# Optimization experiments

Hardware: AMD Instinct MI355X
Metric: run time of the kernel (lower is better)

The kernel has to match this reference:

```python
import jax, jax.numpy as jnp
import numpy as np

B, NQ, ISIZE = 8, 2048, 1024
H, D, NA = 8, 128, 8            # num_head, attn_dim, num_anchor
AH = H * D                      # ahsize = 1024
ASZ = NA * D                    # anchor_size = 1024
FH = 4096                       # _fhsize
ISZ_NET = FH * H // NA          # 4096, input dim of self.net
EPS = 1e-6


def setup_inputs() -> dict:
    key = jax.random.key(0)
    ks = jax.random.split(key, 12)
    def u(k, shape, fan_in):
        s = 1.0 / np.sqrt(fan_in)
        return jax.random.uniform(k, shape, jnp.float32, -s, s)
    return {
        "inputs": jax.random.normal(ks[0], (B, NQ, ISIZE), jnp.float32),
        "ln_g": jnp.ones((ISIZE,), jnp.float32),
        "ln_b": jnp.zeros((ISIZE,), jnp.float32),
        "q_anchor": u(ks[1], (H, NA, D), D),
        "W_qkv": u(ks[2], (ISIZE, 3 * AH), ISIZE), "b_qkv": jnp.zeros((3 * AH,), jnp.float32),
        "W_an": u(ks[3], (ASZ, FH), ASZ), "b_an": jnp.zeros((FH,), jnp.float32),
        "W_n1": u(ks[4], (ISZ_NET, AH), ISZ_NET), "b_n1": jnp.zeros((AH,), jnp.float32),
        "W_n2": u(ks[5], (AH, FH), AH), "b_n2": jnp.zeros((FH,), jnp.float32),
        "W_n3": u(ks[6], (FH, AH), FH), "b_n3": jnp.zeros((AH,), jnp.float32),
        "W_k": u(ks[7], (AH, AH), AH), "b_k": jnp.zeros((AH,), jnp.float32),
        "W_o": u(ks[8], (AH, ISIZE), AH), "b_o": jnp.zeros((ISIZE,), jnp.float32),
    }


def reference(inputs, ln_g, ln_b, q_anchor, W_qkv, b_qkv, W_an, b_an,
              W_n1, b_n1, W_n2, b_n2, W_n3, b_n3, W_k, b_k, W_o, b_o):
    b, nq = inputs.shape[:2]
    scale = 1.0 / np.sqrt(D)
    # pre-LayerNorm
    mu = jnp.mean(inputs, -1, keepdims=True)
    var = jnp.mean(jnp.square(inputs - mu), -1, keepdims=True)
    x = (inputs - mu) * jax.lax.rsqrt(var + EPS) * ln_g + ln_b
    # QKV projection
    qkv = (x @ W_qkv + b_qkv).reshape(b, nq, 3, H, D)
    q = jnp.transpose(qkv[:, :, 0], (0, 2, 1, 3))   # [b,H,nq,D]
    k = qkv[:, :, 1]                                  # [b,nq,H,D]
    v = qkv[:, :, 2]                                  # [b,nq,H,D]
    # stage 1: fixed anchors attend over the sequence
    sc1 = jax.nn.softmax(jnp.einsum('had,bnhd->bhan', q_anchor, k) * scale, axis=-1)
    out = jnp.einsum('bhan,bnhd->bhad', sc1, v).reshape(b, H, ASZ)   # [b,H,NA*D]
    # anchor_net (share_head Linear + ReLU)
    out = jax.nn.relu(out @ W_an + b_an)                              # [b,H,FH]
    # regroup head-major -> anchor-major
    out = out.reshape(b, H, NA, FH // NA).transpose(0, 2, 1, 3).reshape(b, NA, ISZ_NET)
    # net: bottleneck Linear -> Linear -> ReLU -> Linear
    out = jax.nn.relu((out @ W_n1 + b_n1) @ W_n2 + b_n2) @ W_n3 + b_n3  # [b,NA,AH]
    # stage 2: queries attend over anchors
    kk = (out @ W_k + b_k).reshape(b, NA, H, D)
    sc2 = jax.nn.softmax(jnp.einsum('bhqd,bahd->bhqa', q, kk) * scale, axis=-1)
    ov = out.reshape(b, NA, H, D)
    y = jnp.einsum('bhqa,bahd->bqhd', sc2, ov).reshape(b, nq, AH)
    return y @ W_o + b_o + inputs
```

## Files before the change

### kernel.cpp

```cpp
#include <hip/hip_runtime.h>
#include <cstdint>
#include <cstddef>

typedef unsigned short u16;
typedef __attribute__((ext_vector_type(8))) short short8;
typedef __attribute__((ext_vector_type(4))) float floatx4;
typedef __attribute__((ext_vector_type(16))) float floatx16;

__device__ __forceinline__ u16 f2bf(float f) {
  unsigned u = __float_as_uint(f);
  u += 0x7fffu + ((u >> 16) & 1u);
  return (u16)(u >> 16);
}
__device__ __forceinline__ float bf2f(u16 s) {
  return __uint_as_float(((unsigned)s) << 16);
}

__global__ __launch_bounds__(256) void ln_kernel(const float* __restrict__ x,
                                                 const float* __restrict__ g,
                                                 const float* __restrict__ bta,
                                                 u16* __restrict__ out) {
  const int row = blockIdx.x;
  const int tid = threadIdx.x;
  const float4 v = ((const float4*)(x + (size_t)row * 1024))[tid];
  float s = v.x + v.y + v.z + v.w;
#pragma unroll
  for (int o = 32; o > 0; o >>= 1) s += __shfl_down(s, o);
  __shared__ float red[4], red2[4];
  const int wv = tid >> 6, ln = tid & 63;
  if (ln == 0) red[wv] = s;
  __syncthreads();
  const float mean = (red[0] + red[1] + red[2] + red[3]) * (1.0f / 1024.0f);
  const float dx = v.x - mean, dy = v.y - mean, dz = v.z - mean, dw = v.w - mean;
  float s2 = dx * dx + dy * dy + dz * dz + dw * dw;
#pragma unroll
  for (int o = 32; o > 0; o >>= 1) s2 += __shfl_down(s2, o);
  if (ln == 0) red2[wv] = s2;
  __syncthreads();
  const float var = (red2[0] + red2[1] + red2[2] + red2[3]) * (1.0f / 1024.0f);
  const float rstd = rsqrtf(var + 1e-6f);
  const float4 gg = ((const float4*)g)[tid];
  const float4 bb = ((const float4*)bta)[tid];
  ushort4 o4;
  o4.x = f2bf(dx * rstd * gg.x + bb.x);
  o4.y = f2bf(dy * rstd * gg.y + bb.y);
  o4.z = f2bf(dz * rstd * gg.z + bb.z);
  o4.w = f2bf(dw * rstd * gg.w + bb.w);
  ((ushort4*)(out + (size_t)row * 1024))[tid] = o4;
}

__global__ __launch_bounds__(256) void transpose_bf16(const float* __restrict__ W,
                                                      u16* __restrict__ WT,
                                                      int K, int N) {
  __shared__ float t[32][33];
  const int kb = blockIdx.x * 32, nb = blockIdx.y * 32;
  const int tx = threadIdx.x & 31, ty = threadIdx.x >> 5;
#pragma unroll
  for (int i = ty; i < 32; i += 8) t[i][tx] = W[(size_t)(kb + i) * N + nb + tx];
  __syncthreads();
#pragma unroll
  for (int i = ty; i < 32; i += 8) WT[(size_t)(nb + i) * K + kb + tx] = f2bf(t[tx][i]);
}


__device__ __forceinline__ void stageG(const u16* __restrict__ gp, u16* lp, int K) {
  __builtin_amdgcn_global_load_lds((const __attribute__((address_space(1))) void*)gp,
                                   (__attribute__((address_space(3))) void*)lp, 16, 0, 0);
  __builtin_amdgcn_global_load_lds((const __attribute__((address_space(1))) void*)(gp + ((size_t)K << 6)),
                                   (__attribute__((address_space(3))) void*)(lp + 4096), 16, 0, 0);
}

__device__ __forceinline__ void rdA(short8 (&af)[2][4], const u16* sbuf, const int (&ab)[4],
                                    int halfoff) {
#pragma unroll
  for (int mi = 0; mi < 2; ++mi)
#pragma unroll
    for (int ks = 0; ks < 4; ++ks)
      af[mi][ks] = *(const short8*)(sbuf + halfoff + mi * 2048 + ab[ks]);
}
__device__ __forceinline__ void rdB(short8 (&bf)[4], const u16* sbuf, const int (&bb)[4],
                                    int halfoff) {
#pragma unroll
  for (int ks = 0; ks < 4; ++ks)
    bf[ks] = *(const short8*)(sbuf + halfoff + bb[ks]);
}

template <int Q>
__device__ __forceinline__ void mfmaQ(floatx16 (&acc)[4][2], const short8 (&af)[2][4],
                                      const short8 (&bf)[4]) {
#pragma unroll
  for (int ks = 0; ks < 4; ++ks)
#pragma unroll
    for (int mi = 0; mi < 2; ++mi)
      acc[Q][mi] = __builtin_amdgcn_mfma_f32_32x32x16_bf16(af[mi][ks], bf[ks], acc[Q][mi], 0, 0, 0);
}

template <int B_>
__device__ __forceinline__ void gtile(int t, int NT, int K,
                                      u16 (&sA)[2][16384], u16 (&sB)[2][16384],
                                      const u16* gA_lo, const u16* gA_hi,
                                      const u16* gB_lo, const u16* gB_hi,
                                      u16* ldsA_cur, u16* ldsA_alt,
                                      u16* ldsB_cur, u16* ldsB_alt,
                                      const int (&ab)[4], const int (&bb)[4],
                                      floatx16 (&acc)[4][2]) {
  short8 af[2][4], bf0[4], bf1[4];
  rdA(af, sA[B_], ab, 0);
  rdB(bf0, sB[B_], bb, 0);
  __builtin_amdgcn_sched_barrier(0);
  if (t + 1 < NT) stageG(gA_hi + ((t + 1) << 6), ldsA_alt + 8192, K);
  rdB(bf1, sB[B_], bb, 8192);
  asm volatile("s_waitcnt lgkmcnt(4)" ::: "memory");
  __builtin_amdgcn_sched_barrier(0);
  __builtin_amdgcn_s_setprio(1);
  mfmaQ<0>(acc, af, bf0);
  __builtin_amdgcn_s_setprio(0);
  if (t + 1 < NT) stageG(gB_lo + ((t + 1) << 6), ldsB_alt, K);
  asm volatile("s_waitcnt lgkmcnt(0)" ::: "memory");
  __builtin_amdgcn_sched_barrier(0);
  __builtin_amdgcn_s_setprio(1);
  mfmaQ<1>(acc, af, bf1);
  __builtin_amdgcn_s_setprio(0);
  rdA(af, sA[B_], ab, 8192);
  __builtin_amdgcn_s_barrier();
  if (t + 2 < NT) stageG(gA_lo + ((t + 2) << 6), ldsA_cur, K);
  asm volatile("s_waitcnt lgkmcnt(0)" ::: "memory");
  __builtin_amdgcn_sched_barrier(0);
  __builtin_amdgcn_s_setprio(1);
  mfmaQ<2>(acc, af, bf1);
  __builtin_amdgcn_s_setprio(0);
  if (t + 2 < NT) stageG(gB_hi + ((t + 2) << 6), ldsB_cur + 8192, K);
  __builtin_amdgcn_s_setprio(1);
  mfmaQ<3>(acc, af, bf0);
  __builtin_amdgcn_s_setprio(0);
  if (t + 2 < NT) {
    asm volatile("s_waitcnt vmcnt(4)" ::: "memory");
  } else {
    asm volatile("s_waitcnt vmcnt(0)" ::: "memory");
  }
  __builtin_amdgcn_s_barrier();
}

template <int EPI>
__global__ __launch_bounds__(512, 2) void gemm_bf16(const u16* __restrict__ A,
                                                    const u16* __restrict__ BT,
                                                    const float* __restrict__ bias,
                                                    const float* __restrict__ extra,
                                                    u16* __restrict__ outB,
                                                    float* __restrict__ outF,
                                                    int M, int N, int K) {
  __shared__ u16 sA[2][16384];
  __shared__ u16 sB[2][16384];
  const int tid = threadIdx.x;
  const int wave = tid >> 6, lane = tid & 63;
  const int m0 = blockIdx.x * 256, n0 = blockIdx.y * 256;
  const int wr = wave >> 2, wc = wave & 3;
  const int l31 = lane & 31, l5 = lane >> 5, l7 = lane & 7;
  const int NT = K >> 6;

  int ab[4], bb[4];
#pragma unroll
  for (int ks = 0; ks < 4; ++ks) {
    const int xr = ((((ks << 1) + l5) ^ l7) << 3);
    ab[ks] = (wr * 64 + l31) * 64 + xr;
    bb[ks] = (wc * 32 + l31) * 64 + xr;
  }
  const int srow = wave * 8 + (lane >> 3);
  const int scol = ((lane & 7) ^ (srow & 7)) << 3;
  const u16* gA_lo = A + (size_t)(m0 + srow) * K + scol;
  const u16* gA_hi = A + (size_t)(m0 + 128 + srow) * K + scol;
  const u16* gB_lo = BT + (size_t)(n0 + srow) * K + scol;
  const u16* gB_hi = BT + (size_t)(n0 + 128 + srow) * K + scol;

  floatx16 acc[4][2];
#pragma unroll
  for (int q = 0; q < 4; ++q)
#pragma unroll
    for (int mi = 0; mi < 2; ++mi)
#pragma unroll
      for (int r = 0; r < 16; ++r) acc[q][mi][r] = 0.f;

  stageG(gA_lo, &sA[0][0] + wave * 512, K);
  stageG(gA_hi, &sA[0][8192] + wave * 512, K);
  stageG(gB_lo, &sB[0][0] + wave * 512, K);
  stageG(gB_hi, &sB[0][8192] + wave * 512, K);
  stageG(gA_lo + 64, &sA[1][0] + wave * 512, K);
  stageG(gB_hi + 64, &sB[1][8192] + wave * 512, K);
  asm volatile("s_waitcnt vmcnt(4)" ::: "memory");
  __builtin_amdgcn_s_barrier();

  for (int t = 0; t < NT; t += 2) {
    gtile<0>(t, NT, K, sA, sB, gA_lo, gA_hi, gB_lo, gB_hi,
             &sA[0][0] + wave * 512, &sA[1][0] + wave * 512,
             &sB[0][0] + wave * 512, &sB[1][0] + wave * 512, ab, bb, acc);
    gtile<1>(t + 1, NT, K, sA, sB, gA_lo, gA_hi, gB_lo, gB_hi,
             &sA[1][0] + wave * 512, &sA[0][0] + wave * 512,
             &sB[1][0] + wave * 512, &sB[0][0] + wave * 512, ab, bb, acc);
  }

#pragma unroll
  for (int q = 0; q < 4; ++q) {
    const int QM = q >> 1, QN = QM ^ (q & 1);
    const int n = n0 + QN * 128 + wc * 32 + l31;
    const float bs = bias[n];
#pragma unroll
    for (int mi = 0; mi < 2; ++mi) {
      const int mb = m0 + QM * 128 + wr * 64 + mi * 32 + 4 * l5;
#pragma unroll
      for (int reg = 0; reg < 16; ++reg) {
        const int m = mb + (reg & 3) + 8 * (reg >> 2);
        const float v = acc[q][mi][reg] + bs;
        if (EPI == 0)
          outB[(size_t)m * N + n] = f2bf(v);
        else
          outF[(size_t)m * N + n] = v + extra[(size_t)m * N + n];
      }
    }
  }
}

__global__ __launch_bounds__(256) void attn1_scores(const u16* __restrict__ qkv,
                                                    const float* __restrict__ q_anchor,
                                                    float* __restrict__ S) {
  __shared__ float qa[8][128];
  const int tid = threadIdx.x;
  const int chunk = blockIdx.x & 7, bh = blockIdx.x >> 3;
  const int b = bh >> 3, h = bh & 7;
  for (int i = tid; i < 1024; i += 256) qa[i >> 7][i & 127] = q_anchor[h * 1024 + i];
  __syncthreads();
  const float scale = 0.0883883476483184f;
  const int n = chunk * 256 + tid;
  const u16* kp = qkv + (size_t)(b * 2048 + n) * 3072 + 1024 + h * 128;
  float dots[8] = {0, 0, 0, 0, 0, 0, 0, 0};
#pragma unroll 8
  for (int dd = 0; dd < 128; dd += 4) {
    const ushort4 k4 = *(const ushort4*)(kp + dd);
    const float k0 = bf2f(k4.x), k1 = bf2f(k4.y), k2 = bf2f(k4.z), k3 = bf2f(k4.w);
#pragma unroll
    for (int a = 0; a < 8; ++a) {
      const float4 q4 = *(const float4*)&qa[a][dd];
      dots[a] += q4.x * k0 + q4.y * k1 + q4.z * k2 + q4.w * k3;
    }
  }
#pragma unroll
  for (int a = 0; a < 8; ++a) S[((size_t)(bh * 8 + a)) * 2048 + n] = dots[a] * scale;
}

__global__ __launch_bounds__(256) void attn1_softmax(float* __restrict__ S) {
  const int row = blockIdx.x;
  const int tid = threadIdx.x;
  float* Sp = S + (size_t)row * 2048;
  float4 v0 = ((const float4*)Sp)[tid * 2];
  float4 v1 = ((const float4*)Sp)[tid * 2 + 1];
  float mx = fmaxf(fmaxf(fmaxf(v0.x, v0.y), fmaxf(v0.z, v0.w)),
                   fmaxf(fmaxf(v1.x, v1.y), fmaxf(v1.z, v1.w)));
#pragma unroll
  for (int o = 32; o > 0; o >>= 1) mx = fmaxf(mx, __shfl_xor(mx, o));
  __shared__ float red[4];
  const int wv = tid >> 6, ln = tid & 63;
  if (ln == 0) red[wv] = mx;
  __syncthreads();
  mx = fmaxf(fmaxf(red[0], red[1]), fmaxf(red[2], red[3]));
  v0.x = __expf(v0.x - mx); v0.y = __expf(v0.y - mx);
  v0.z = __expf(v0.z - mx); v0.w = __expf(v0.w - mx);
  v1.x = __expf(v1.x - mx); v1.y = __expf(v1.y - mx);
  v1.z = __expf(v1.z - mx); v1.w = __expf(v1.w - mx);
  float sum = v0.x + v0.y + v0.z + v0.w + v1.x + v1.y + v1.z + v1.w;
#pragma unroll
  for (int o = 32; o > 0; o >>= 1) sum += __shfl_xor(sum, o);
  __shared__ float red2[4];
  if (ln == 0) red2[wv] = sum;
  __syncthreads();
  const float inv = 1.f / (red2[0] + red2[1] + red2[2] + red2[3]);
  v0.x *= inv; v0.y *= inv; v0.z *= inv; v0.w *= inv;
  v1.x *= inv; v1.y *= inv; v1.z *= inv; v1.w *= inv;
  ((float4*)Sp)[tid * 2] = v0;
  ((float4*)Sp)[tid * 2 + 1] = v1;
}

__global__ __launch_bounds__(256) void attn1_pv(const u16* __restrict__ qkv,
                                                const float* __restrict__ S,
                                                float* __restrict__ pvpart) {
  __shared__ float P[8][256];
  const int tid = threadIdx.x;
  const int chunk = blockIdx.x & 7, bh = blockIdx.x >> 3;
  const int b = bh >> 3, h = bh & 7;
  for (int i = tid; i < 2048; i += 256) {
    const int a = i >> 8, n = i & 255;
    P[a][n] = S[((size_t)(bh * 8 + a)) * 2048 + chunk * 256 + n];
  }
  __syncthreads();
  const int d = tid & 127, half = tid >> 7;
  const int nbase = chunk * 256 + half * 128;
  const u16* vp = qkv + (size_t)(b * 2048 + nbase) * 3072 + 2048 + h * 128 + d;
  float acc[8] = {0.f};
  for (int n = 0; n < 128; n += 4) {
    const float v0 = bf2f(vp[(size_t)n * 3072]);
    const float v1 = bf2f(vp[(size_t)(n + 1) * 3072]);
    const float v2 = bf2f(vp[(size_t)(n + 2) * 3072]);
    const float v3 = bf2f(vp[(size_t)(n + 3) * 3072]);
#pragma unroll
    for (int a = 0; a < 8; ++a) {
      const float4 s4 = *(const float4*)&P[a][half * 128 + n];
      acc[a] += s4.x * v0 + s4.y * v1 + s4.z * v2 + s4.w * v3;
    }
  }
  const int split = chunk * 2 + half;
#pragma unroll
  for (int a = 0; a < 8; ++a)
    pvpart[((size_t)split * 64 + bh) * 1024 + a * 128 + d] = acc[a];
}

__global__ __launch_bounds__(256) void mlp_mfma(const float* __restrict__ A,
                                                const float* __restrict__ W,
                                                float* __restrict__ part,
                                                int K, int N, int KC) {
  __shared__ float sW[64][33];
  const int tid = threadIdx.x;
  const int lane = tid & 63, wave = tid >> 6;
  const int wm = wave * 16;
  const int n0 = blockIdx.x * 64;
  const int kbeg = blockIdx.y * KC;
  const int l15 = lane & 15, kq8 = (lane >> 4) * 8;
  const int arow = wm + l15;

  floatx4 acc[4];
  const floatx4 zero = {0.f, 0.f, 0.f, 0.f};
#pragma unroll
  for (int j = 0; j < 4; ++j) acc[j] = zero;

  for (int kc = 0; kc < KC; kc += 32) {
    const int kbase = kbeg + kc;
    __syncthreads();
#pragma unroll
    for (int p = 0; p < 8; ++p) {
      const int k = p * 4 + wave;
      sW[lane][k] = W[(size_t)(kbase + k) * N + n0 + lane];
    }
    const float* ap = A + (size_t)arow * K + kbase + kq8;
    const float4 a0 = *(const float4*)ap;
    const float4 a1 = *(const float4*)(ap + 4);
    short8 af;
    af[0] = (short)f2bf(a0.x); af[1] = (short)f2bf(a0.y);
    af[2] = (short)f2bf(a0.z); af[3] = (short)f2bf(a0.w);
    af[4] = (short)f2bf(a1.x); af[5] = (short)f2bf(a1.y);
    af[6] = (short)f2bf(a1.z); af[7] = (short)f2bf(a1.w);
    __syncthreads();
#pragma unroll
    for (int j = 0; j < 4; ++j) {
      const float* wp = &sW[j * 16 + l15][kq8];
      short8 bf;
      bf[0] = (short)f2bf(wp[0]); bf[1] = (short)f2bf(wp[1]);
      bf[2] = (short)f2bf(wp[2]); bf[3] = (short)f2bf(wp[3]);
      bf[4] = (short)f2bf(wp[4]); bf[5] = (short)f2bf(wp[5]);
      bf[6] = (short)f2bf(wp[6]); bf[7] = (short)f2bf(wp[7]);
      acc[j] = __builtin_amdgcn_mfma_f32_16x16x32_bf16(af, bf, acc[j], 0, 0, 0);
    }
  }
  const int q = lane >> 4;
#pragma unroll
  for (int j = 0; j < 4; ++j)
#pragma unroll
    for (int r = 0; r < 4; ++r) {
      const int m = wm + q * 4 + r;
      const int n = n0 + j * 16 + l15;
      part[((size_t)blockIdx.y * 64 + m) * N + n] = acc[j][r];
    }
}

__global__ __launch_bounds__(256) void mlp_reduce(const float* __restrict__ part,
                                                  const float* __restrict__ bias,
                                                  float* __restrict__ out,
                                                  int N, int nsplit, int relu, int perm) {
  const int idx = blockIdx.x * 256 + threadIdx.x;
  const int e = idx * 4;
  if (e >= 64 * N) return;
  const int row = e / N, col = e - row * N;
  float4 acc;
  if (bias) acc = *(const float4*)&bias[col];
  else { acc.x = 0.f; acc.y = 0.f; acc.z = 0.f; acc.w = 0.f; }
  for (int s = 0; s < nsplit; ++s) {
    const float4 p = *(const float4*)&part[((size_t)s * 64 + row) * N + col];
    acc.x += p.x; acc.y += p.y; acc.z += p.z; acc.w += p.w;
  }
  if (relu) {
    acc.x = fmaxf(acc.x, 0.f); acc.y = fmaxf(acc.y, 0.f);
    acc.z = fmaxf(acc.z, 0.f); acc.w = fmaxf(acc.w, 0.f);
  }
  size_t oidx;
  if (!perm) {
    oidx = (size_t)row * N + col;
  } else {
    const int b = row >> 3, h = row & 7;
    oidx = (size_t)(b * 8 + (col >> 9)) * 4096 + h * 512 + (col & 511);
  }
  *(float4*)&out[oidx] = acc;
}

__global__ __launch_bounds__(256) void attn2_kernel(const u16* __restrict__ qkv,
                                                    const float* __restrict__ kk,
                                                    const float* __restrict__ onet,
                                                    u16* __restrict__ y) {
  __shared__ float kkl[8][128];
  __shared__ float ovl[8][128];
  const int tid = threadIdx.x;
  const int chunk = blockIdx.x & 7, bh = blockIdx.x >> 3;
  const int b = bh >> 3, h = bh & 7;
  for (int i = tid; i < 1024; i += 256) {
    const int a = i >> 7, d = i & 127;
    kkl[a][d] = kk[(size_t)(b * 8 + a) * 1024 + h * 128 + d];
    ovl[a][d] = onet[(size_t)(b * 8 + a) * 1024 + h * 128 + d];
  }
  __syncthreads();
  const int n = chunk * 256 + tid;
  const u16* qp = qkv + (size_t)(b * 2048 + n) * 3072 + h * 128;
  float dots[8] = {0, 0, 0, 0, 0, 0, 0, 0};
#pragma unroll 4
  for (int dd = 0; dd < 128; dd += 4) {
    const ushort4 q4 = *(const ushort4*)(qp + dd);
    const float q0 = bf2f(q4.x), q1 = bf2f(q4.y), q2 = bf2f(q4.z), q3 = bf2f(q4.w);
#pragma unroll
    for (int a = 0; a < 8; ++a) {
      const float4 k4 = *(const float4*)&kkl[a][dd];
      dots[a] += k4.x * q0 + k4.y * q1 + k4.z * q2 + k4.w * q3;
    }
  }
  const float scale = 0.0883883476483184f;
  float mx = -1e30f;
#pragma unroll
  for (int a = 0; a < 8; ++a) {
    dots[a] *= scale;
    mx = fmaxf(mx, dots[a]);
  }
  float p[8];
  float sum = 0.f;
#pragma unroll
  for (int a = 0; a < 8; ++a) {
    p[a] = __expf(dots[a] - mx);
    sum += p[a];
  }
  const float inv = 1.f / sum;
#pragma unroll
  for (int a = 0; a < 8; ++a) p[a] *= inv;
  u16* yp = y + (size_t)(b * 2048 + n) * 1024 + h * 128;
#pragma unroll 4
  for (int dd = 0; dd < 128; dd += 4) {
    float a0 = 0, a1 = 0, a2 = 0, a3 = 0;
#pragma unroll
    for (int a = 0; a < 8; ++a) {
      const float4 o4 = *(const float4*)&ovl[a][dd];
      a0 += p[a] * o4.x;
      a1 += p[a] * o4.y;
      a2 += p[a] * o4.z;
      a3 += p[a] * o4.w;
    }
    ushort4 o;
    o.x = f2bf(a0);
    o.y = f2bf(a1);
    o.z = f2bf(a2);
    o.w = f2bf(a3);
    *(ushort4*)(yp + dd) = o;
  }
}

extern "C" void kernel_launch(void* const* d_in, const int* in_sizes, int n_in,
                              void* d_out, int out_size, void* d_ws, size_t ws_size,
                              hipStream_t stream) {
  const float* inputs = (const float*)d_in[0];
  const float* ln_g = (const float*)d_in[1];
  const float* ln_b = (const float*)d_in[2];
  const float* q_anchor = (const float*)d_in[3];
  const float* W_qkv = (const float*)d_in[4];
  const float* b_qkv = (const float*)d_in[5];
  const float* W_an = (const float*)d_in[6];
  const float* b_an = (const float*)d_in[7];
  const float* W_n1 = (const float*)d_in[8];
  const float* b_n1 = (const float*)d_in[9];
  const float* W_n2 = (const float*)d_in[10];
  const float* b_n2 = (const float*)d_in[11];
  const float* W_n3 = (const float*)d_in[12];
  const float* b_n3 = (const float*)d_in[13];
  const float* W_k = (const float*)d_in[14];
  const float* b_k = (const float*)d_in[15];
  const float* W_o = (const float*)d_in[16];
  const float* b_o = (const float*)d_in[17];
  float* out = (float*)d_out;

  char* ws = (char*)d_ws;
  u16* qkv = (u16*)(ws);
  u16* xbf = (u16*)(ws + 100663296);
  float* S = (float*)(ws + 100663296);
  float* part = (float*)(ws + 109051904);
  u16* WqkvT = (u16*)(ws + 134217728);
  u16* WoT = (u16*)(ws + 140509184);
  float* att1 = (float*)(ws + 142606336);
  float* anp = (float*)(ws + 142868480);
  float* h1 = (float*)(ws + 143917056);
  float* h2 = (float*)(ws + 144179200);
  float* onet = (float*)(ws + 145227776);
  float* kkb = (float*)(ws + 145489920);

  ln_kernel<<<16384, 256, 0, stream>>>(inputs, ln_g, ln_b, xbf);
  transpose_bf16<<<dim3(32, 96), 256, 0, stream>>>(W_qkv, WqkvT, 1024, 3072);
  transpose_bf16<<<dim3(32, 32), 256, 0, stream>>>(W_o, WoT, 1024, 1024);
  gemm_bf16<0><<<dim3(64, 12), 512, 0, stream>>>(xbf, WqkvT, b_qkv, nullptr, qkv, nullptr,
                                                 16384, 3072, 1024);
  attn1_scores<<<512, 256, 0, stream>>>(qkv, q_anchor, S);
  attn1_softmax<<<512, 256, 0, stream>>>(S);
  attn1_pv<<<512, 256, 0, stream>>>(qkv, S, part);
  mlp_reduce<<<64, 256, 0, stream>>>(part, nullptr, att1, 1024, 16, 0, 0);
  mlp_mfma<<<dim3(64, 8), 256, 0, stream>>>(att1, W_an, part, 1024, 4096, 128);
  mlp_reduce<<<256, 256, 0, stream>>>(part, b_an, anp, 4096, 8, 1, 1);
  mlp_mfma<<<dim3(16, 32), 256, 0, stream>>>(anp, W_n1, part, 4096, 1024, 128);
  mlp_reduce<<<64, 256, 0, stream>>>(part, b_n1, h1, 1024, 32, 0, 0);
  mlp_mfma<<<dim3(64, 8), 256, 0, stream>>>(h1, W_n2, part, 1024, 4096, 128);
  mlp_reduce<<<256, 256, 0, stream>>>(part, b_n2, h2, 4096, 8, 1, 0);
  mlp_mfma<<<dim3(16, 32), 256, 0, stream>>>(h2, W_n3, part, 4096, 1024, 128);
  mlp_reduce<<<64, 256, 0, stream>>>(part, b_n3, onet, 1024, 32, 0, 0);
  mlp_mfma<<<dim3(16, 16), 256, 0, stream>>>(onet, W_k, part, 1024, 1024, 64);
  mlp_reduce<<<64, 256, 0, stream>>>(part, b_k, kkb, 1024, 16, 0, 0);
  attn2_kernel<<<512, 256, 0, stream>>>(qkv, kkb, onet, xbf);
  gemm_bf16<1><<<dim3(64, 4), 512, 0, stream>>>(xbf, WoT, b_o, inputs, nullptr, out,
                                                16384, 1024, 1024);
}
```

Measured before the change: 601.3 us.

## Change LDS swizzle and prefetch next tile's B fragments across the barrier

The GEMM's LDS XOR swizzle now also folds in the wave index and row group, with a per-mi XOR on A reads, to reduce bank conflicts on the ds_read paths. The main loop also carries B fragments across iterations: the low-half B fragments of the next tile are read after the barrier and before the last MFMA quarter. The two B register sets swap roles between tiles, so the reads overlap with compute instead of stalling at the start of each tile. This raises register pressure and depends on the staged writes and swizzled reads agreeing exactly.

```diff
diff --git a/kernel.cpp b/kernel.cpp
--- a/kernel.cpp
+++ b/kernel.cpp
@@ -76,7 +76,7 @@
   for (int mi = 0; mi < 2; ++mi)
 #pragma unroll
     for (int ks = 0; ks < 4; ++ks)
-      af[mi][ks] = *(const short8*)(sbuf + halfoff + mi * 2048 + ab[ks]);
+      af[mi][ks] = *(const short8*)(sbuf + halfoff + mi * 2048 + (ab[ks] ^ (mi << 5)));
 }
 __device__ __forceinline__ void rdB(short8 (&bf)[4], const u16* sbuf, const int (&bb)[4],
                                     int halfoff) {
@@ -103,42 +103,43 @@
                                       u16* ldsA_cur, u16* ldsA_alt,
                                       u16* ldsB_cur, u16* ldsB_alt,
                                       const int (&ab)[4], const int (&bb)[4],
-                                      floatx16 (&acc)[4][2]) {
-  short8 af[2][4], bf0[4], bf1[4];
-  rdA(af, sA[B_], ab, 0);
-  rdB(bf0, sB[B_], bb, 0);
+                                      floatx16 (&acc)[4][2],
+                                      short8 (&afA)[2][4], short8 (&bfP)[4], short8 (&bfN)[4]) {
+  rdA(afA, sA[B_], ab, 0);
   __builtin_amdgcn_sched_barrier(0);
   if (t + 1 < NT) stageG(gA_hi + ((t + 1) << 6), ldsA_alt + 8192, K);
-  rdB(bf1, sB[B_], bb, 8192);
+  rdB(bfN, sB[B_], bb, 8192);
   asm volatile("s_waitcnt lgkmcnt(4)" ::: "memory");
   __builtin_amdgcn_sched_barrier(0);
   __builtin_amdgcn_s_setprio(1);
-  mfmaQ<0>(acc, af, bf0);
+  mfmaQ<0>(acc, afA, bfP);
   __builtin_amdgcn_s_setprio(0);
   if (t + 1 < NT) stageG(gB_lo + ((t + 1) << 6), ldsB_alt, K);
   asm volatile("s_waitcnt lgkmcnt(0)" ::: "memory");
   __builtin_amdgcn_sched_barrier(0);
   __builtin_amdgcn_s_setprio(1);
-  mfmaQ<1>(acc, af, bf1);
+  mfmaQ<1>(acc, afA, bfN);
   __builtin_amdgcn_s_setprio(0);
-  rdA(af, sA[B_], ab, 8192);
+  rdA(afA, sA[B_], ab, 8192);
   __builtin_amdgcn_s_barrier();
   if (t + 2 < NT) stageG(gA_lo + ((t + 2) << 6), ldsA_cur, K);
   asm volatile("s_waitcnt lgkmcnt(0)" ::: "memory");
   __builtin_amdgcn_sched_barrier(0);
   __builtin_amdgcn_s_setprio(1);
-  mfmaQ<2>(acc, af, bf1);
+  mfmaQ<2>(acc, afA, bfN);
   __builtin_amdgcn_s_setprio(0);
   if (t + 2 < NT) stageG(gB_hi + ((t + 2) << 6), ldsB_cur + 8192, K);
-  __builtin_amdgcn_s_setprio(1);
-  mfmaQ<3>(acc, af, bf0);
-  __builtin_amdgcn_s_setprio(0);
   if (t + 2 < NT) {
     asm volatile("s_waitcnt vmcnt(4)" ::: "memory");
   } else {
     asm volatile("s_waitcnt vmcnt(0)" ::: "memory");
   }
   __builtin_amdgcn_s_barrier();
+  if (t + 1 < NT) rdB(bfN, sB[B_ ^ 1], bb, 0);
+  __builtin_amdgcn_sched_barrier(0);
+  __builtin_amdgcn_s_setprio(1);
+  mfmaQ<3>(acc, afA, bfP);
+  __builtin_amdgcn_s_setprio(0);
 }
 
 template <int EPI>
@@ -158,15 +159,17 @@
   const int l31 = lane & 31, l5 = lane >> 5, l7 = lane & 7;
   const int NT = K >> 6;
 
+  const int fa = l7 ^ (l31 >> 3);
+  const int fb = l7 ^ ((wc * 4 + (l31 >> 3)) & 7);
   int ab[4], bb[4];
 #pragma unroll
   for (int ks = 0; ks < 4; ++ks) {
-    const int xr = ((((ks << 1) + l5) ^ l7) << 3);
-    ab[ks] = (wr * 64 + l31) * 64 + xr;
-    bb[ks] = (wc * 32 + l31) * 64 + xr;
+    const int kg = (ks << 1) + l5;
+    ab[ks] = (wr * 64 + l31) * 64 + (((kg ^ fa) & 7) << 3);
+    bb[ks] = (wc * 32 + l31) * 64 + (((kg ^ fb) & 7) << 3);
   }
   const int srow = wave * 8 + (lane >> 3);
-  const int scol = ((lane & 7) ^ (srow & 7)) << 3;
+  const int scol = ((lane & 7) ^ (lane >> 3) ^ wave) << 3;
   const u16* gA_lo = A + (size_t)(m0 + srow) * K + scol;
   const u16* gA_hi = A + (size_t)(m0 + 128 + srow) * K + scol;
   const u16* gB_lo = BT + (size_t)(n0 + srow) * K + scol;
@@ -189,13 +192,17 @@
   asm volatile("s_waitcnt vmcnt(4)" ::: "memory");
   __builtin_amdgcn_s_barrier();
 
+  short8 afA[2][4], bfX[4], bfY[4];
+  rdB(bfX, sB[0], bb, 0);
+  __builtin_amdgcn_sched_barrier(0);
+
   for (int t = 0; t < NT; t += 2) {
     gtile<0>(t, NT, K, sA, sB, gA_lo, gA_hi, gB_lo, gB_hi,
              &sA[0][0] + wave * 512, &sA[1][0] + wave * 512,
-             &sB[0][0] + wave * 512, &sB[1][0] + wave * 512, ab, bb, acc);
+             &sB[0][0] + wave * 512, &sB[1][0] + wave * 512, ab, bb, acc, afA, bfX, bfY);
     gtile<1>(t + 1, NT, K, sA, sB, gA_lo, gA_hi, gB_lo, gB_hi,
              &sA[1][0] + wave * 512, &sA[0][0] + wave * 512,
-             &sB[1][0] + wave * 512, &sB[0][0] + wave * 512, ab, bb, acc);
+             &sB[1][0] + wave * 512, &sB[0][0] + wave * 512, ab, bb, acc, afA, bfY, bfX);
   }
 
 #pragma unroll
```

New measurement: 587.1 us. -2.4%, faster.
